# Kernel tuning notes

Measured on AMD Instinct MI355X. Metric: run time of the kernel, lower is better.

The kernel has to match this reference:

```python
import jax, jax.numpy as jnp
import numpy as np


def setup_inputs() -> dict:
    key = jax.random.key(0)
    kx, ka, kw, kb = jax.random.split(key, 4)
    B, N, IN, OUT = 4, 4096, 128, 128
    X = jax.random.normal(kx, (B, N, IN), dtype=jnp.float32)
    A = jax.random.uniform(ka, (B, N, N), dtype=jnp.float32)
    # nn.Linear(in_dim, out_dim): W is [out_dim, in_dim], b is [out_dim]
    bound = 1.0 / np.sqrt(IN)
    W = jax.random.uniform(kw, (OUT, IN), dtype=jnp.float32, minval=-bound, maxval=bound)
    b = jax.random.uniform(kb, (OUT,), dtype=jnp.float32, minval=-bound, maxval=bound)
    return {"X": X, "A": A, "W": W, "b": b}


def reference(X, A, W, b):
    B, N, _ = X.shape
    # A_hat = A + I (self loops)
    A_hat = A + jnp.eye(N, dtype=A.dtype)[None, :, :]
    deg = A_hat.sum(-1)  # [B, N]
    d_inv_sqrt = jnp.where(deg > 0, jax.lax.rsqrt(deg), 0.0)  # inf -> 0 as in torch code
    # D^{-1/2} A_hat D^{-1/2}: diag bmms are row/col scaling (same math, no N^3 diag GEMMs)
    A_norm = d_inv_sqrt[:, :, None] * A_hat * d_inv_sqrt[:, None, :]
    H = jnp.einsum('bnm,bmd->bnd', A_norm, X)  # propagation
    return jnp.einsum('bnd,od->bno', H, W) + b  # linear
```

## Files before the change

### kernel.cpp

```cpp
#include <hip/hip_runtime.h>
#include <hip/hip_bf16.h>
#include <stdint.h>

#define BB 4
#define NN 4096
#define DD 128
#define BK 128

typedef __attribute__((ext_vector_type(8))) short short8;
typedef __attribute__((ext_vector_type(4))) float f32x4;

static __device__ __forceinline__ unsigned short f2bf(float f) {
  unsigned u = __builtin_bit_cast(unsigned, f);
  u += 0x7fffu + ((u >> 16) & 1u);
  return (unsigned short)(u >> 16);
}

__global__ __launch_bounds__(256) void k_deg(const float* __restrict__ A,
                                             float* __restrict__ dinv) {
  const int row = blockIdx.x;
  const float* a = A + (size_t)row * NN;
  float s = 0.f;
  for (int i = threadIdx.x * 4; i < NN; i += 256 * 4) {
    const float4 v = *reinterpret_cast<const float4*>(a + i);
    s += (v.x + v.y) + (v.z + v.w);
  }
  for (int off = 32; off > 0; off >>= 1) s += __shfl_down(s, off, 64);
  __shared__ float red[4];
  if ((threadIdx.x & 63) == 0) red[threadIdx.x >> 6] = s;
  __syncthreads();
  if (threadIdx.x == 0) {
    const float deg = (red[0] + red[1]) + (red[2] + red[3]) + 1.0f;
    dinv[row] = 1.0f / sqrtf(deg);
  }
}

__global__ __launch_bounds__(256) void k_prep(const float* __restrict__ X,
                                              const float* __restrict__ dinv,
                                              unsigned short* __restrict__ Yt) {
  __shared__ unsigned short tile[64][130];
  const int b = blockIdx.x >> 6;
  const int m0 = (blockIdx.x & 63) << 6;
  const float* Xb = X + ((size_t)b * NN + m0) * DD;
  const float* dv = dinv + b * NN + m0;
  for (int idx = threadIdx.x; idx < 64 * 128; idx += 256) {
    const int mi = idx >> 7, d = idx & 127;
    tile[mi][d] = f2bf(Xb[mi * DD + d] * dv[mi]);
  }
  __syncthreads();
  for (int idx = threadIdx.x; idx < 128 * 64; idx += 256) {
    const int d = idx >> 6, j = idx & 63;
    Yt[((size_t)b * DD + d) * NN + m0 + j] = tile[j][d];
  }
}

__global__ __launch_bounds__(256) void k_w(const float* __restrict__ W,
                                           unsigned short* __restrict__ Wb) {
  int idx = blockIdx.x * 1024 + threadIdx.x;
  for (int k = 0; k < 4; ++k, idx += 256) Wb[idx] = f2bf(W[idx]);
}

__global__ __launch_bounds__(512) void k_main(const float* __restrict__ A,
                                              const unsigned short* __restrict__ Yt,
                                              const unsigned short* __restrict__ Wb,
                                              const float* __restrict__ X,
                                              const float* __restrict__ dinv,
                                              const float* __restrict__ bias,
                                              float* __restrict__ out) {
  __shared__ char lds[98304];

  const int tid = threadIdx.x;
  const int l   = tid & 63;
  const int wid = tid >> 6;
  const int b   = blockIdx.x >> 6;
  const int n0  = (blockIdx.x & 63) << 6;
  const int wr  = wid >> 2;
  const int wc  = wid & 3;

  const float* Ab = A + (size_t)(b * NN + n0) * NN;
  const unsigned short* Ytb = Yt + (size_t)b * DD * NN;

  const int sar = tid >> 3;
  const int sg0 = (tid & 7) << 1;
  const float* pA = Ab + (size_t)sar * NN + (sg0 << 3);
  float4 ra[4];
  auto LOADA = [&](int t) {
#pragma unroll
    for (int i = 0; i < 4; ++i)
      ra[i] = *reinterpret_cast<const float4*>(pA + t * BK + i * 4);
  };
  auto CVTA = [&](int nb) {
    char* As = lds + nb * 49152 + sar * 256;
#pragma unroll
    for (int j = 0; j < 2; ++j) {
      short8 v;
      v[0] = (short)f2bf(ra[2*j].x);   v[1] = (short)f2bf(ra[2*j].y);
      v[2] = (short)f2bf(ra[2*j].z);   v[3] = (short)f2bf(ra[2*j].w);
      v[4] = (short)f2bf(ra[2*j+1].x); v[5] = (short)f2bf(ra[2*j+1].y);
      v[6] = (short)f2bf(ra[2*j+1].z); v[7] = (short)f2bf(ra[2*j+1].w);
      *reinterpret_cast<short8*>(As + (((sg0 + j) ^ (sar & 15)) << 4)) = v;
    }
  };

  const int glrow4 = l >> 4;
  const int glslot = l & 15;
  auto GLDS = [&](const unsigned short* src, int rstride, int colh, char* dstBase) {
#pragma unroll
    for (int i = 0; i < 4; ++i) {
      const int rloc = wid * 16 + i * 4 + glrow4;
      const int g = glslot ^ ((i * 4 + glrow4) & 15);
      __builtin_amdgcn_global_load_lds(src + (size_t)rloc * rstride + colh + g * 8,
                                       dstBase + (wid * 16 + i * 4) * 256, 16, 0, 0);
    }
  };

  const int lrow = l & 15;
  const int lg   = l >> 4;
  const int ar0 = wr * 32 + lrow, ar1 = ar0 + 16;
  const int br0 = wc * 32 + lrow, br1 = br0 + 16;

  f32x4 acc[2][2] = {};
  auto GEMMSTEP = [&](int nb, f32x4 (&ac)[2][2]) {
    const char* Ap = lds + nb * 49152;
    const char* Bp = Ap + 16384;
#pragma unroll
    for (int kc = 0; kc < 4; ++kc) {
      const int g = kc * 4 + lg;
      const short8 a0 = *reinterpret_cast<const short8*>(Ap + ar0 * 256 + ((g ^ (ar0 & 15)) << 4));
      const short8 a1 = *reinterpret_cast<const short8*>(Ap + ar1 * 256 + ((g ^ (ar1 & 15)) << 4));
      const short8 b0 = *reinterpret_cast<const short8*>(Bp + br0 * 256 + ((g ^ (br0 & 15)) << 4));
      const short8 b1 = *reinterpret_cast<const short8*>(Bp + br1 * 256 + ((g ^ (br1 & 15)) << 4));
      ac[0][0] = __builtin_amdgcn_mfma_f32_16x16x32_bf16(a0, b0, ac[0][0], 0, 0, 0);
      ac[0][1] = __builtin_amdgcn_mfma_f32_16x16x32_bf16(a0, b1, ac[0][1], 0, 0, 0);
      ac[1][0] = __builtin_amdgcn_mfma_f32_16x16x32_bf16(a1, b0, ac[1][0], 0, 0, 0);
      ac[1][1] = __builtin_amdgcn_mfma_f32_16x16x32_bf16(a1, b1, ac[1][1], 0, 0, 0);
    }
  };

  LOADA(0);
  GLDS(Ytb, NN, 0, lds + 16384);
  asm volatile("s_waitcnt vmcnt(4)" ::: "memory");
  CVTA(0);
  LOADA(1);
  GLDS(Ytb, NN, BK, lds + 49152 + 16384);
  asm volatile("s_waitcnt vmcnt(8) lgkmcnt(0)" ::: "memory");
  __builtin_amdgcn_s_barrier();

  const int NT = NN / BK;
  for (int t = 0; t < NT; ++t) {
    const int cur = t & 1;
    asm volatile("s_waitcnt vmcnt(4)" ::: "memory");
    CVTA(cur ^ 1);
    GEMMSTEP(cur, acc);
    asm volatile("s_waitcnt vmcnt(0) lgkmcnt(0)" ::: "memory");
    __builtin_amdgcn_s_barrier();
    const int tn = (t + 2 < NT) ? t + 2 : NT - 1;
    LOADA(tn);
    GLDS(Ytb, NN, tn * BK, lds + cur * 49152 + 16384);
  }

  const int rg = lg << 2;
  const float* Xb  = X + (size_t)(b * NN + n0) * DD;
  const float* dvb = dinv + b * NN + n0;
#pragma unroll
  for (int mi = 0; mi < 2; ++mi)
#pragma unroll
    for (int r = 0; r < 4; ++r) {
      const int nl = wr * 32 + mi * 16 + rg + r;
      const float dn = dvb[nl];
#pragma unroll
      for (int ni = 0; ni < 2; ++ni) {
        const int d = wc * 32 + ni * 16 + lrow;
        const float h = dn * (acc[mi][ni][r] + dn * Xb[nl * DD + d]);
        *reinterpret_cast<unsigned short*>(
            lds + nl * 256 + (((d >> 3) ^ (nl & 15)) << 4) + (d & 7) * 2) = f2bf(h);
      }
    }
  GLDS(Wb, DD, 0, lds + 16384);
  asm volatile("s_waitcnt vmcnt(0) lgkmcnt(0)" ::: "memory");
  __builtin_amdgcn_s_barrier();

  f32x4 acc2[2][2] = {};
  GEMMSTEP(0, acc2);

  float* outb = out + (size_t)(b * NN + n0) * DD;
#pragma unroll
  for (int ni = 0; ni < 2; ++ni) {
    const int o = wc * 32 + ni * 16 + lrow;
    const float bo = bias[o];
#pragma unroll
    for (int mi = 0; mi < 2; ++mi)
#pragma unroll
      for (int r = 0; r < 4; ++r) {
        const int nl = wr * 32 + mi * 16 + rg + r;
        outb[(size_t)nl * DD + o] = acc2[mi][ni][r] + bo;
      }
  }
}

extern "C" void kernel_launch(void* const* d_in, const int* in_sizes, int n_in,
                              void* d_out, int out_size, void* d_ws, size_t ws_size,
                              hipStream_t stream) {
  const float* X    = (const float*)d_in[0];
  const float* A    = (const float*)d_in[1];
  const float* W    = (const float*)d_in[2];
  const float* bias = (const float*)d_in[3];
  float* out = (float*)d_out;

  char* ws = (char*)d_ws;
  float* dinv = (float*)ws;
  unsigned short* Yt = (unsigned short*)(ws + 65536);
  unsigned short* Wb = Yt + (size_t)BB * DD * NN;

  k_deg <<<BB * NN, 256, 0, stream>>>(A, dinv);
  k_w   <<<16, 256, 0, stream>>>(W, Wb);
  k_prep<<<BB * (NN / 64), 256, 0, stream>>>(X, dinv, Yt);
  k_main<<<BB * (NN / 64), 512, 0, stream>>>(A, Yt, Wb, X, dinv, bias, out);
}
```

Measured before the change: 122.9 us.

## Shrink main GEMM tile to 32 rows with smaller K step and register-staged loads

The main propagation kernel now uses 32-row output tiles with 256 threads and BK=64. This doubles the grid to 512 blocks, and the smaller LDS footprint allows two blocks per CU. The async global-to-LDS loads for Yt are replaced with register-staged loads and plain __syncthreads double buffering. The second GEMM now reads W directly from global memory instead of staging it in LDS. The intent is more occupancy and parallelism, at the cost of reading Yt twice as often per row of A and losing the hand-tuned waitcnt pipelining.

```diff
diff --git a/kernel.cpp b/kernel.cpp
--- a/kernel.cpp
+++ b/kernel.cpp
@@ -5,7 +5,8 @@
 #define BB 4
 #define NN 4096
 #define DD 128
-#define BK 128
+#define BM 32
+#define BK 64
 
 typedef __attribute__((ext_vector_type(8))) short short8;
 typedef __attribute__((ext_vector_type(4))) float f32x4;
@@ -60,103 +61,92 @@
   for (int k = 0; k < 4; ++k, idx += 256) Wb[idx] = f2bf(W[idx]);
 }
 
-__global__ __launch_bounds__(512) void k_main(const float* __restrict__ A,
-                                              const unsigned short* __restrict__ Yt,
-                                              const unsigned short* __restrict__ Wb,
-                                              const float* __restrict__ X,
-                                              const float* __restrict__ dinv,
-                                              const float* __restrict__ bias,
-                                              float* __restrict__ out) {
-  __shared__ char lds[98304];
+__global__ __launch_bounds__(256, 2) void k_main(const float* __restrict__ A,
+                                                 const unsigned short* __restrict__ Yt,
+                                                 const unsigned short* __restrict__ Wb,
+                                                 const float* __restrict__ X,
+                                                 const float* __restrict__ dinv,
+                                                 const float* __restrict__ bias,
+                                                 float* __restrict__ out) {
+  __shared__ char lds[40960];
 
   const int tid = threadIdx.x;
   const int l   = tid & 63;
   const int wid = tid >> 6;
-  const int b   = blockIdx.x >> 6;
-  const int n0  = (blockIdx.x & 63) << 6;
-  const int wr  = wid >> 2;
-  const int wc  = wid & 3;
+  const int b   = blockIdx.x >> 7;
+  const int n0  = (blockIdx.x & 127) << 5;
 
   const float* Ab = A + (size_t)(b * NN + n0) * NN;
   const unsigned short* Ytb = Yt + (size_t)b * DD * NN;
 
   const int sar = tid >> 3;
-  const int sg0 = (tid & 7) << 1;
-  const float* pA = Ab + (size_t)sar * NN + (sg0 << 3);
-  float4 ra[4];
+  const int sag = tid & 7;
+  const float* pA = Ab + (size_t)sar * NN + sag * 8;
+  float4 ra0, ra1;
   auto LOADA = [&](int t) {
-#pragma unroll
-    for (int i = 0; i < 4; ++i)
-      ra[i] = *reinterpret_cast<const float4*>(pA + t * BK + i * 4);
-  };
-  auto CVTA = [&](int nb) {
-    char* As = lds + nb * 49152 + sar * 256;
-#pragma unroll
-    for (int j = 0; j < 2; ++j) {
-      short8 v;
-      v[0] = (short)f2bf(ra[2*j].x);   v[1] = (short)f2bf(ra[2*j].y);
-      v[2] = (short)f2bf(ra[2*j].z);   v[3] = (short)f2bf(ra[2*j].w);
-      v[4] = (short)f2bf(ra[2*j+1].x); v[5] = (short)f2bf(ra[2*j+1].y);
-      v[6] = (short)f2bf(ra[2*j+1].z); v[7] = (short)f2bf(ra[2*j+1].w);
-      *reinterpret_cast<short8*>(As + (((sg0 + j) ^ (sar & 15)) << 4)) = v;
-    }
-  };
-
-  const int glrow4 = l >> 4;
-  const int glslot = l & 15;
-  auto GLDS = [&](const unsigned short* src, int rstride, int colh, char* dstBase) {
-#pragma unroll
-    for (int i = 0; i < 4; ++i) {
-      const int rloc = wid * 16 + i * 4 + glrow4;
-      const int g = glslot ^ ((i * 4 + glrow4) & 15);
-      __builtin_amdgcn_global_load_lds(src + (size_t)rloc * rstride + colh + g * 8,
-                                       dstBase + (wid * 16 + i * 4) * 256, 16, 0, 0);
-    }
+    ra0 = *reinterpret_cast<const float4*>(pA + t * BK);
+    ra1 = *reinterpret_cast<const float4*>(pA + t * BK + 4);
+  };
+  auto WRITEA = [&](int nb) {
+    short8 v;
+    v[0] = (short)f2bf(ra0.x); v[1] = (short)f2bf(ra0.y);
+    v[2] = (short)f2bf(ra0.z); v[3] = (short)f2bf(ra0.w);
+    v[4] = (short)f2bf(ra1.x); v[5] = (short)f2bf(ra1.y);
+    v[6] = (short)f2bf(ra1.z); v[7] = (short)f2bf(ra1.w);
+    *reinterpret_cast<short8*>(lds + nb * 20480 + sar * 128 + ((sag ^ (sar & 7)) << 4)) = v;
+  };
+
+  const int yrow = tid >> 1;
+  const int yg0  = (tid & 1) << 2;
+  const unsigned short* pY = Ytb + (size_t)yrow * NN + yg0 * 8;
+  uint4 ry[4];
+  auto LOADB = [&](int t) {
+#pragma unroll
+    for (int j = 0; j < 4; ++j)
+      ry[j] = *reinterpret_cast<const uint4*>(pY + t * BK + j * 8);
+  };
+  auto WRITEB = [&](int nb) {
+    char* Bs = lds + nb * 20480 + 4096 + yrow * 128;
+#pragma unroll
+    for (int j = 0; j < 4; ++j)
+      *reinterpret_cast<uint4*>(Bs + (((yg0 + j) ^ (yrow & 7)) << 4)) = ry[j];
   };
 
   const int lrow = l & 15;
   const int lg   = l >> 4;
-  const int ar0 = wr * 32 + lrow, ar1 = ar0 + 16;
-  const int br0 = wc * 32 + lrow, br1 = br0 + 16;
+  const int ar0 = lrow, ar1 = lrow + 16;
+  const int br0 = wid * 32 + lrow, br1 = br0 + 16;
 
   f32x4 acc[2][2] = {};
-  auto GEMMSTEP = [&](int nb, f32x4 (&ac)[2][2]) {
-    const char* Ap = lds + nb * 49152;
-    const char* Bp = Ap + 16384;
-#pragma unroll
-    for (int kc = 0; kc < 4; ++kc) {
+  auto GEMMSTEP = [&](int nb) {
+    const char* Ap = lds + nb * 20480;
+    const char* Bp = Ap + 4096;
+#pragma unroll
+    for (int kc = 0; kc < 2; ++kc) {
       const int g = kc * 4 + lg;
-      const short8 a0 = *reinterpret_cast<const short8*>(Ap + ar0 * 256 + ((g ^ (ar0 & 15)) << 4));
-      const short8 a1 = *reinterpret_cast<const short8*>(Ap + ar1 * 256 + ((g ^ (ar1 & 15)) << 4));
-      const short8 b0 = *reinterpret_cast<const short8*>(Bp + br0 * 256 + ((g ^ (br0 & 15)) << 4));
-      const short8 b1 = *reinterpret_cast<const short8*>(Bp + br1 * 256 + ((g ^ (br1 & 15)) << 4));
-      ac[0][0] = __builtin_amdgcn_mfma_f32_16x16x32_bf16(a0, b0, ac[0][0], 0, 0, 0);
-      ac[0][1] = __builtin_amdgcn_mfma_f32_16x16x32_bf16(a0, b1, ac[0][1], 0, 0, 0);
-      ac[1][0] = __builtin_amdgcn_mfma_f32_16x16x32_bf16(a1, b0, ac[1][0], 0, 0, 0);
-      ac[1][1] = __builtin_amdgcn_mfma_f32_16x16x32_bf16(a1, b1, ac[1][1], 0, 0, 0);
+      const short8 a0 = *reinterpret_cast<const short8*>(Ap + ar0 * 128 + ((g ^ (ar0 & 7)) << 4));
+      const short8 a1 = *reinterpret_cast<const short8*>(Ap + ar1 * 128 + ((g ^ (ar1 & 7)) << 4));
+      const short8 b0 = *reinterpret_cast<const short8*>(Bp + br0 * 128 + ((g ^ (br0 & 7)) << 4));
+      const short8 b1 = *reinterpret_cast<const short8*>(Bp + br1 * 128 + ((g ^ (br1 & 7)) << 4));
+      acc[0][0] = __builtin_amdgcn_mfma_f32_16x16x32_bf16(a0, b0, acc[0][0], 0, 0, 0);
+      acc[0][1] = __builtin_amdgcn_mfma_f32_16x16x32_bf16(a0, b1, acc[0][1], 0, 0, 0);
+      acc[1][0] = __builtin_amdgcn_mfma_f32_16x16x32_bf16(a1, b0, acc[1][0], 0, 0, 0);
+      acc[1][1] = __builtin_amdgcn_mfma_f32_16x16x32_bf16(a1, b1, acc[1][1], 0, 0, 0);
     }
   };
 
-  LOADA(0);
-  GLDS(Ytb, NN, 0, lds + 16384);
-  asm volatile("s_waitcnt vmcnt(4)" ::: "memory");
-  CVTA(0);
-  LOADA(1);
-  GLDS(Ytb, NN, BK, lds + 49152 + 16384);
-  asm volatile("s_waitcnt vmcnt(8) lgkmcnt(0)" ::: "memory");
-  __builtin_amdgcn_s_barrier();
-
+  LOADA(0); LOADB(0);
+  WRITEA(0); WRITEB(0);
+  __syncthreads();
+
+  int cur = 0;
   const int NT = NN / BK;
   for (int t = 0; t < NT; ++t) {
-    const int cur = t & 1;
-    asm volatile("s_waitcnt vmcnt(4)" ::: "memory");
-    CVTA(cur ^ 1);
-    GEMMSTEP(cur, acc);
-    asm volatile("s_waitcnt vmcnt(0) lgkmcnt(0)" ::: "memory");
-    __builtin_amdgcn_s_barrier();
-    const int tn = (t + 2 < NT) ? t + 2 : NT - 1;
-    LOADA(tn);
-    GLDS(Ytb, NN, tn * BK, lds + cur * 49152 + 16384);
+    if (t + 1 < NT) { LOADA(t + 1); LOADB(t + 1); }
+    GEMMSTEP(cur);
+    if (t + 1 < NT) { WRITEA(cur ^ 1); WRITEB(cur ^ 1); }
+    __syncthreads();
+    cur ^= 1;
   }
 
   const int rg = lg << 2;
@@ -166,33 +156,42 @@
   for (int mi = 0; mi < 2; ++mi)
 #pragma unroll
     for (int r = 0; r < 4; ++r) {
-      const int nl = wr * 32 + mi * 16 + rg + r;
+      const int nl = mi * 16 + rg + r;
       const float dn = dvb[nl];
 #pragma unroll
       for (int ni = 0; ni < 2; ++ni) {
-        const int d = wc * 32 + ni * 16 + lrow;
+        const int d = wid * 32 + ni * 16 + lrow;
         const float h = dn * (acc[mi][ni][r] + dn * Xb[nl * DD + d]);
         *reinterpret_cast<unsigned short*>(
             lds + nl * 256 + (((d >> 3) ^ (nl & 15)) << 4) + (d & 7) * 2) = f2bf(h);
       }
     }
-  GLDS(Wb, DD, 0, lds + 16384);
-  asm volatile("s_waitcnt vmcnt(0) lgkmcnt(0)" ::: "memory");
-  __builtin_amdgcn_s_barrier();
+  __syncthreads();
 
   f32x4 acc2[2][2] = {};
-  GEMMSTEP(0, acc2);
+#pragma unroll
+  for (int kc = 0; kc < 4; ++kc) {
+    const int g = kc * 4 + lg;
+    const short8 a0 = *reinterpret_cast<const short8*>(lds + ar0 * 256 + ((g ^ (ar0 & 15)) << 4));
+    const short8 a1 = *reinterpret_cast<const short8*>(lds + ar1 * 256 + ((g ^ (ar1 & 15)) << 4));
+    const short8 b0 = *reinterpret_cast<const short8*>(Wb + br0 * DD + g * 8);
+    const short8 b1 = *reinterpret_cast<const short8*>(Wb + br1 * DD + g * 8);
+    acc2[0][0] = __builtin_amdgcn_mfma_f32_16x16x32_bf16(a0, b0, acc2[0][0], 0, 0, 0);
+    acc2[0][1] = __builtin_amdgcn_mfma_f32_16x16x32_bf16(a0, b1, acc2[0][1], 0, 0, 0);
+    acc2[1][0] = __builtin_amdgcn_mfma_f32_16x16x32_bf16(a1, b0, acc2[1][0], 0, 0, 0);
+    acc2[1][1] = __builtin_amdgcn_mfma_f32_16x16x32_bf16(a1, b1, acc2[1][1], 0, 0, 0);
+  }
 
   float* outb = out + (size_t)(b * NN + n0) * DD;
 #pragma unroll
   for (int ni = 0; ni < 2; ++ni) {
-    const int o = wc * 32 + ni * 16 + lrow;
+    const int o = wid * 32 + ni * 16 + lrow;
     const float bo = bias[o];
 #pragma unroll
     for (int mi = 0; mi < 2; ++mi)
 #pragma unroll
       for (int r = 0; r < 4; ++r) {
-        const int nl = wr * 32 + mi * 16 + rg + r;
+        const int nl = mi * 16 + rg + r;
         outb[(size_t)nl * DD + o] = acc2[mi][ni][r] + bo;
       }
   }
@@ -215,5 +214,5 @@
   k_deg <<<BB * NN, 256, 0, stream>>>(A, dinv);
   k_w   <<<16, 256, 0, stream>>>(W, Wb);
   k_prep<<<BB * (NN / 64), 256, 0, stream>>>(X, dinv, Yt);
-  k_main<<<BB * (NN / 64), 512, 0, stream>>>(A, Yt, Wb, X, dinv, bias, out);
-}
+  k_main<<<BB * (NN / BM), 256, 0, stream>>>(A, Yt, Wb, X, dinv, bias, out);
+}
```

Measured after the change: 189.2 us. +53.9%, slower.

## Triple-buffer main loop with smaller K tile and staggered K start

Applied to the files above, without the earlier changes.

The main propagation loop now uses a 64-wide K tile with three rotating LDS buffers for A and Yt instead of two 128-wide buffers, so loads for two tiles ahead stay in flight while the current tile is computed. Each block starts its K traversal at a different offset (blockIdx*29 mod 64) to spread concurrent accesses across memory channels. The final W GEMM reads W directly from global memory instead of staging it through LDS, and LDS usage drops, which may allow better occupancy. The risks are more barriers per unit of work, shorter MFMA bursts per barrier, and uncoalesced global reads of W in the epilogue.

```diff
diff --git a/kernel.cpp b/kernel.cpp
--- a/kernel.cpp
+++ b/kernel.cpp
@@ -5,7 +5,7 @@
 #define BB 4
 #define NN 4096
 #define DD 128
-#define BK 128
+#define BK 64
 
 typedef __attribute__((ext_vector_type(8))) short short8;
 typedef __attribute__((ext_vector_type(4))) float f32x4;
@@ -67,7 +67,7 @@
                                               const float* __restrict__ dinv,
                                               const float* __restrict__ bias,
                                               float* __restrict__ out) {
-  __shared__ char lds[98304];
+  __shared__ char lds[73728];
 
   const int tid = threadIdx.x;
   const int l   = tid & 63;
@@ -76,43 +76,20 @@
   const int n0  = (blockIdx.x & 63) << 6;
   const int wr  = wid >> 2;
   const int wc  = wid & 3;
+  const int phase = (blockIdx.x * 29) & 63;
 
   const float* Ab = A + (size_t)(b * NN + n0) * NN;
   const unsigned short* Ytb = Yt + (size_t)b * DD * NN;
 
   const int sar = tid >> 3;
-  const int sg0 = (tid & 7) << 1;
-  const float* pA = Ab + (size_t)sar * NN + (sg0 << 3);
-  float4 ra[4];
-  auto LOADA = [&](int t) {
-#pragma unroll
-    for (int i = 0; i < 4; ++i)
-      ra[i] = *reinterpret_cast<const float4*>(pA + t * BK + i * 4);
-  };
-  auto CVTA = [&](int nb) {
-    char* As = lds + nb * 49152 + sar * 256;
-#pragma unroll
-    for (int j = 0; j < 2; ++j) {
-      short8 v;
-      v[0] = (short)f2bf(ra[2*j].x);   v[1] = (short)f2bf(ra[2*j].y);
-      v[2] = (short)f2bf(ra[2*j].z);   v[3] = (short)f2bf(ra[2*j].w);
-      v[4] = (short)f2bf(ra[2*j+1].x); v[5] = (short)f2bf(ra[2*j+1].y);
-      v[6] = (short)f2bf(ra[2*j+1].z); v[7] = (short)f2bf(ra[2*j+1].w);
-      *reinterpret_cast<short8*>(As + (((sg0 + j) ^ (sar & 15)) << 4)) = v;
-    }
-  };
-
-  const int glrow4 = l >> 4;
-  const int glslot = l & 15;
-  auto GLDS = [&](const unsigned short* src, int rstride, int colh, char* dstBase) {
-#pragma unroll
-    for (int i = 0; i < 4; ++i) {
-      const int rloc = wid * 16 + i * 4 + glrow4;
-      const int g = glslot ^ ((i * 4 + glrow4) & 15);
-      __builtin_amdgcn_global_load_lds(src + (size_t)rloc * rstride + colh + g * 8,
-                                       dstBase + (wid * 16 + i * 4) * 256, 16, 0, 0);
-    }
-  };
+  const int sag = tid & 7;
+  const float* pA = Ab + (size_t)sar * NN + sag * 8;
+  const int awrel = sar * 128 + ((sag ^ (sar & 7)) << 4);
+
+  const int brow = wid * 16 + (l >> 3);
+  const int bgr  = ((l & 7) ^ (l >> 3)) << 3;
+  const unsigned short* pB0 = Ytb + (size_t)brow * NN + bgr;
+  const unsigned short* pB1 = Ytb + (size_t)(brow + 8) * NN + bgr;
 
   const int lrow = l & 15;
   const int lg   = l >> 4;
@@ -120,43 +97,76 @@
   const int br0 = wc * 32 + lrow, br1 = br0 + 16;
 
   f32x4 acc[2][2] = {};
-  auto GEMMSTEP = [&](int nb, f32x4 (&ac)[2][2]) {
-    const char* Ap = lds + nb * 49152;
-    const char* Bp = Ap + 16384;
-#pragma unroll
-    for (int kc = 0; kc < 4; ++kc) {
-      const int g = kc * 4 + lg;
-      const short8 a0 = *reinterpret_cast<const short8*>(Ap + ar0 * 256 + ((g ^ (ar0 & 15)) << 4));
-      const short8 a1 = *reinterpret_cast<const short8*>(Ap + ar1 * 256 + ((g ^ (ar1 & 15)) << 4));
-      const short8 b0 = *reinterpret_cast<const short8*>(Bp + br0 * 256 + ((g ^ (br0 & 15)) << 4));
-      const short8 b1 = *reinterpret_cast<const short8*>(Bp + br1 * 256 + ((g ^ (br1 & 15)) << 4));
-      ac[0][0] = __builtin_amdgcn_mfma_f32_16x16x32_bf16(a0, b0, ac[0][0], 0, 0, 0);
-      ac[0][1] = __builtin_amdgcn_mfma_f32_16x16x32_bf16(a0, b1, ac[0][1], 0, 0, 0);
-      ac[1][0] = __builtin_amdgcn_mfma_f32_16x16x32_bf16(a1, b0, ac[1][0], 0, 0, 0);
-      ac[1][1] = __builtin_amdgcn_mfma_f32_16x16x32_bf16(a1, b1, ac[1][1], 0, 0, 0);
-    }
-  };
-
-  LOADA(0);
-  GLDS(Ytb, NN, 0, lds + 16384);
-  asm volatile("s_waitcnt vmcnt(4)" ::: "memory");
-  CVTA(0);
-  LOADA(1);
-  GLDS(Ytb, NN, BK, lds + 49152 + 16384);
-  asm volatile("s_waitcnt vmcnt(8) lgkmcnt(0)" ::: "memory");
-  __builtin_amdgcn_s_barrier();
-
+
+#define TPH(t) (((t) + phase) & 63)
+#define LOADA(t, s0, s1)                                                    \
+  { const int c_ = TPH(t) * BK;                                             \
+    s0 = *reinterpret_cast<const float4*>(pA + c_);                         \
+    s1 = *reinterpret_cast<const float4*>(pA + c_ + 4); }
+#define GLDSB(t, boff)                                                      \
+  { const size_t c_ = (size_t)TPH(t) * BK;                                  \
+    char* d_ = lds + (boff) + wid * 2048;                                   \
+    __builtin_amdgcn_global_load_lds(pB0 + c_, d_, 16, 0, 0);               \
+    __builtin_amdgcn_global_load_lds(pB1 + c_, d_ + 1024, 16, 0, 0); }
+#define CVTA(s0, s1, aoff)                                                  \
+  { short8 v_;                                                              \
+    v_[0] = (short)f2bf(s0.x); v_[1] = (short)f2bf(s0.y);                   \
+    v_[2] = (short)f2bf(s0.z); v_[3] = (short)f2bf(s0.w);                   \
+    v_[4] = (short)f2bf(s1.x); v_[5] = (short)f2bf(s1.y);                   \
+    v_[6] = (short)f2bf(s1.z); v_[7] = (short)f2bf(s1.w);                   \
+    *reinterpret_cast<short8*>(lds + (aoff) + awrel) = v_; }
+#define GEMMSTEP(aoff, boff)                                                \
+  { const char* Ap_ = lds + (aoff);                                         \
+    const char* Bp_ = lds + (boff);                                         \
+    _Pragma("unroll")                                                       \
+    for (int kc = 0; kc < 2; ++kc) {                                        \
+      const int g_ = kc * 4 + lg;                                           \
+      const short8 a0 = *reinterpret_cast<const short8*>(Ap_ + ar0 * 128 + ((g_ ^ (ar0 & 7)) << 4)); \
+      const short8 a1 = *reinterpret_cast<const short8*>(Ap_ + ar1 * 128 + ((g_ ^ (ar1 & 7)) << 4)); \
+      const short8 b0 = *reinterpret_cast<const short8*>(Bp_ + br0 * 128 + ((g_ ^ (br0 & 7)) << 4)); \
+      const short8 b1 = *reinterpret_cast<const short8*>(Bp_ + br1 * 128 + ((g_ ^ (br1 & 7)) << 4)); \
+      acc[0][0] = __builtin_amdgcn_mfma_f32_16x16x32_bf16(a0, b0, acc[0][0], 0, 0, 0); \
+      acc[0][1] = __builtin_amdgcn_mfma_f32_16x16x32_bf16(a0, b1, acc[0][1], 0, 0, 0); \
+      acc[1][0] = __builtin_amdgcn_mfma_f32_16x16x32_bf16(a1, b0, acc[1][0], 0, 0, 0); \
+      acc[1][1] = __builtin_amdgcn_mfma_f32_16x16x32_bf16(a1, b1, acc[1][1], 0, 0, 0); } }
+#define VMCNT4   asm volatile("s_waitcnt vmcnt(4)" ::: "memory")
+#define LGKM0    asm volatile("s_waitcnt lgkmcnt(0)" ::: "memory")
+#define BARRIER  { __builtin_amdgcn_s_barrier(); __builtin_amdgcn_sched_barrier(0); }
+
+  float4 e0, e1, o0, o1;
   const int NT = NN / BK;
-  for (int t = 0; t < NT; ++t) {
-    const int cur = t & 1;
-    asm volatile("s_waitcnt vmcnt(4)" ::: "memory");
-    CVTA(cur ^ 1);
-    GEMMSTEP(cur, acc);
-    asm volatile("s_waitcnt vmcnt(0) lgkmcnt(0)" ::: "memory");
-    __builtin_amdgcn_s_barrier();
-    const int tn = (t + 2 < NT) ? t + 2 : NT - 1;
-    LOADA(tn);
-    GLDS(Ytb, NN, tn * BK, lds + cur * 49152 + 16384);
+
+  LOADA(0, e0, e1);
+  GLDSB(0, 24576);
+  LOADA(1, o0, o1);
+  GLDSB(1, 24576 + 16384);
+  VMCNT4;
+  CVTA(e0, e1, 0);
+  LGKM0;
+  BARRIER;
+
+  int a0o = 0, a1o = 8192, a2o = 16384;
+  int b0o = 24576, b1o = 24576 + 16384, b2o = 24576 + 32768;
+
+  for (int t = 0; t < NT; t += 2) {
+    { const int tn = (t + 2 < NT) ? t + 2 : NT - 1;
+      LOADA(tn, e0, e1);
+      GLDSB(tn, b2o); }
+    GEMMSTEP(a0o, b0o);
+    VMCNT4;
+    CVTA(o0, o1, a1o);
+    LGKM0;
+    BARRIER;
+    { const int tn = (t + 3 < NT) ? t + 3 : NT - 1;
+      LOADA(tn, o0, o1);
+      GLDSB(tn, b0o); }
+    GEMMSTEP(a1o, b1o);
+    VMCNT4;
+    CVTA(e0, e1, a2o);
+    LGKM0;
+    BARRIER;
+    int ta = a0o; a0o = a2o; a2o = a1o; a1o = ta;
+    int tb = b0o; b0o = b2o; b2o = b1o; b1o = tb;
   }
 
   const int rg = lg << 2;
@@ -176,12 +186,22 @@
             lds + nl * 256 + (((d >> 3) ^ (nl & 15)) << 4) + (d & 7) * 2) = f2bf(h);
       }
     }
-  GLDS(Wb, DD, 0, lds + 16384);
-  asm volatile("s_waitcnt vmcnt(0) lgkmcnt(0)" ::: "memory");
-  __builtin_amdgcn_s_barrier();
+  LGKM0;
+  BARRIER;
 
   f32x4 acc2[2][2] = {};
-  GEMMSTEP(0, acc2);
+#pragma unroll
+  for (int kc = 0; kc < 4; ++kc) {
+    const int g = kc * 4 + lg;
+    const short8 a0 = *reinterpret_cast<const short8*>(lds + ar0 * 256 + ((g ^ (ar0 & 15)) << 4));
+    const short8 a1 = *reinterpret_cast<const short8*>(lds + ar1 * 256 + ((g ^ (ar1 & 15)) << 4));
+    const short8 b0 = *reinterpret_cast<const short8*>(Wb + br0 * DD + g * 8);
+    const short8 b1 = *reinterpret_cast<const short8*>(Wb + br1 * DD + g * 8);
+    acc2[0][0] = __builtin_amdgcn_mfma_f32_16x16x32_bf16(a0, b0, acc2[0][0], 0, 0, 0);
+    acc2[0][1] = __builtin_amdgcn_mfma_f32_16x16x32_bf16(a0, b1, acc2[0][1], 0, 0, 0);
+    acc2[1][0] = __builtin_amdgcn_mfma_f32_16x16x32_bf16(a1, b0, acc2[1][0], 0, 0, 0);
+    acc2[1][1] = __builtin_amdgcn_mfma_f32_16x16x32_bf16(a1, b1, acc2[1][1], 0, 0, 0);
+  }
 
   float* outb = out + (size_t)(b * NN + n0) * DD;
 #pragma unroll
@@ -196,6 +216,14 @@
         outb[(size_t)nl * DD + o] = acc2[mi][ni][r] + bo;
       }
   }
+#undef TPH
+#undef LOADA
+#undef GLDSB
+#undef CVTA
+#undef GEMMSTEP
+#undef VMCNT4
+#undef LGKM0
+#undef BARRIER
 }
 
 extern "C" void kernel_launch(void* const* d_in, const int* in_sizes, int n_in,
```

After: 131.4 us. +6.9%, slower.
